# Kernel tuning notes

Measured on AMD Instinct MI355X. Metric: run time of the kernel, lower is better.

Reference implementation:

```python
import jax, jax.numpy as jnp
import numpy as np

B = 4
C = 128           # input channels
H = W = 512       # image size
P = 16            # patch size
GH = GW = 32      # token grid (H//P, W//P)
N = GH * GW       # num patches = 1024
PATCH_DIM = C * P * P  # 32768
DIM = 512         # embed dim
MLP = 256         # ffn hidden
DH = 64           # dim per head
HEADS = (2, 4, 8) # per-layer head counts
NUM_REL = (2 * GH - 1) * (2 * GW - 1)  # 3969


def _rel_index():
    # faithful to the torch buffer construction (meshgrid default 'ij')
    coords = np.stack(np.meshgrid(np.arange(GH), np.arange(GW), indexing='ij')).reshape(2, -1)
    rc = (coords[:, :, None] - coords[:, None, :]).transpose(1, 2, 0)  # [N,N,2]
    rc[..., 0] += GH - 1
    rc[..., 1] += GW - 1
    rc[..., 0] *= 2 * GH - 1
    return jnp.asarray(rc.sum(-1))  # [N,N] int

REL_IDX = _rel_index()


def _ln(x, s, b):
    m = x.mean(-1, keepdims=True)
    v = x.var(-1, keepdims=True)
    return (x - m) / jnp.sqrt(v + 1e-5) * s + b


def setup_inputs() -> dict:
    key = jax.random.key(0)
    ks = iter(jax.random.split(key, 40))
    def rn(shape, scale=0.02):
        return jax.random.normal(next(ks), shape, jnp.float32) * scale
    inp = {"img": jax.random.normal(next(ks), (B, C, H, W), jnp.float32)}
    inp["patch_w"] = rn((PATCH_DIM, DIM))
    inp["patch_b"] = jnp.zeros((DIM,), jnp.float32)
    inp["pos_emb"] = rn((1, N, DIM), 1.0)
    inp["ln1_s"] = jnp.ones((3, DIM), jnp.float32)
    inp["ln1_b"] = jnp.zeros((3, DIM), jnp.float32)
    inp["ln2_s"] = jnp.ones((3, DIM), jnp.float32)
    inp["ln2_b"] = jnp.zeros((3, DIM), jnp.float32)
    for l, h in enumerate(HEADS):
        inner = DH * h
        inp[f"qkv_w{l}"] = rn((DIM, 3 * inner))
        inp[f"out_w{l}"] = rn((inner, DIM))
        inp[f"out_b{l}"] = jnp.zeros((DIM,), jnp.float32)
        inp[f"bias{l}"] = rn((NUM_REL, h))
    inp["ff_w1"] = rn((3, DIM, MLP))
    inp["ff_b1"] = jnp.zeros((3, MLP), jnp.float32)
    inp["ff_w2"] = rn((3, MLP, DIM))
    inp["ff_b2"] = jnp.zeros((3, DIM), jnp.float32)
    return inp


def reference(img, patch_w, patch_b, pos_emb, ln1_s, ln1_b, ln2_s, ln2_b,
              qkv_w0, qkv_w1, qkv_w2, out_w0, out_w1, out_w2,
              out_b0, out_b1, out_b2, bias0, bias1, bias2,
              ff_w1, ff_b1, ff_w2, ff_b2):
    b = img.shape[0]
    # Rearrange 'b c (h p1) (w p2) -> b (h w) (p1 p2 c)'
    x = img.reshape(b, C, GH, P, GW, P).transpose(0, 2, 4, 3, 5, 1).reshape(b, N, PATCH_DIM)
    x = x @ patch_w + patch_b + pos_emb

    qkv_ws = (qkv_w0, qkv_w1, qkv_w2)
    out_ws = (out_w0, out_w1, out_w2)
    out_bs = (out_b0, out_b1, out_b2)
    tables = (bias0, bias1, bias2)

    for l, h in enumerate(HEADS):
        # attention with relative position bias
        xn = _ln(x, ln1_s[l], ln1_b[l])
        qkv = xn @ qkv_ws[l]                                  # [b, N, 3*h*DH]
        q, k, v = jnp.split(qkv, 3, axis=-1)
        q = q.reshape(b, N, h, DH).transpose(0, 2, 1, 3)      # bhnd
        k = k.reshape(b, N, h, DH).transpose(0, 2, 1, 3)
        v = v.reshape(b, N, h, DH).transpose(0, 2, 1, 3)
        dots = jnp.einsum('bhnd,bhmd->bhnm', q, k) * (DH ** -0.5)
        rel = tables[l][REL_IDX].transpose(2, 0, 1)           # [h, N, N]
        attn = jax.nn.softmax(dots + rel[None], axis=-1)
        o = jnp.einsum('bhnm,bhmd->bhnd', attn, v)
        o = o.transpose(0, 2, 1, 3).reshape(b, N, h * DH)
        x = o @ out_ws[l] + out_bs[l] + x
        # feed-forward
        xn = _ln(x, ln2_s[l], ln2_b[l])
        hmid = jax.nn.gelu(xn @ ff_w1[l] + ff_b1[l], approximate=False)
        x = hmid @ ff_w2[l] + ff_b2[l] + x

    return x.transpose(0, 2, 1).reshape(b, DIM, GH, GW)
```

## Files before the change

kernel.cpp:

```cpp
#include <hip/hip_runtime.h>

typedef unsigned short u16;
typedef __bf16 bf16x8 __attribute__((ext_vector_type(8)));
typedef float f32x4 __attribute__((ext_vector_type(4)));

#define AS1 __attribute__((address_space(1)))
#define AS3 __attribute__((address_space(3)))
#define MFMA(a,b,c) __builtin_amdgcn_mfma_f32_16x16x32_bf16(a,b,c,0,0,0)

__device__ __forceinline__ u16 f2bf(float f) {
    union { float f; unsigned u; } x; x.f = f;
    unsigned r = x.u + 0x7fffu + ((x.u >> 16) & 1u);
    return (u16)(r >> 16);
}

__global__ void k_patch_wT(const float* __restrict__ w, u16* __restrict__ o)
{
    __shared__ u16 T[256*33];
    int c = blockIdx.x, n0 = blockIdx.y*32;
    int t = threadIdx.x;
    int rr = t >> 5, cc = t & 31;
    #pragma unroll
    for (int i = 0; i < 32; ++i) {
        int r = i*8 + rr;
        int k = (r >> 4)*2048 + (r & 15)*128 + c;
        T[r*33 + cc] = f2bf(w[(size_t)k*512 + n0 + cc]);
    }
    __syncthreads();
    #pragma unroll
    for (int i = 0; i < 4; ++i) {
        int j  = i*8 + (t >> 5);
        int ch = t & 31;
        union { u16 u[8]; uint4 v; } pk;
        #pragma unroll
        for (int q = 0; q < 8; ++q) pk.u[q] = T[(ch*8+q)*33 + j];
        *(uint4*)(o + (size_t)(n0 + j)*32768 + c*256 + ch*8) = pk.v;
    }
}

__global__ void k_init_x(float* __restrict__ x, const float* __restrict__ pb, const float* __restrict__ pe)
{
    int i4 = blockIdx.x*256 + threadIdx.x;
    size_t base = (size_t)i4*4;
    float4 a = *(const float4*)(pb + (base & 511));
    float4 b = *(const float4*)(pe + (base & 524287));
    float4 r = make_float4(a.x+b.x, a.y+b.y, a.z+b.z, a.w+b.w);
    *(float4*)(x + base) = r;
}

struct TXJob { const float* in; u16* out; int K, N, tiles; };
struct TXArgs { TXJob j[12]; };

__global__ void k_wT_all(TXArgs a)
{
    __shared__ float T[32*33];
    int bid = blockIdx.x;
    int ji = 0;
    while (bid >= a.j[ji].tiles) { bid -= a.j[ji].tiles; ++ji; }
    const float* __restrict__ in = a.j[ji].in;
    u16* __restrict__ o = a.j[ji].out;
    const int K = a.j[ji].K, N = a.j[ji].N;
    const int tn = N >> 5;
    const int kt = (bid / tn) * 32, nt = (bid % tn) * 32;
    int t = threadIdx.x, r = t >> 5, c = t & 31;
    #pragma unroll
    for (int i = 0; i < 4; ++i)
        T[(r + i*8)*33 + c] = in[(size_t)(kt + r + i*8)*N + nt + c];
    __syncthreads();
    #pragma unroll
    for (int i = 0; i < 4; ++i)
        o[(size_t)(nt + r + i*8)*K + kt + c] = f2bf(T[c*33 + r + i*8]);
}

__global__ __launch_bounds__(1024) void k_patch_gemm(
    const float* __restrict__ img, const u16* __restrict__ Bt, float* __restrict__ Cf)
{
    __shared__ alignas(16) u16 As[2*128*64];
    __shared__ alignas(16) u16 Bs[2*512*64];
    const int t = threadIdx.x;
    const int bid = blockIdx.x;
    const int z = bid & 7;
    const int tile = bid >> 3;
    const int b = tile >> 3, gh0 = (tile & 7)*4;
    const int m0 = tile*128;
    const int wave = t >> 6, lane = t & 63;
    const int r16 = lane & 15, g = lane >> 4;
    const int wm = (wave >> 3)*64, wn = (wave & 7)*64;

    const int arow = t >> 6;
    const int ghl = arow >> 2, p1l = arow & 3;
    const int aw = (t & 63)*8;
    const int tok = ghl*32 + (aw >> 4);
    unsigned abyte = (unsigned)(tok*128 + p1l*32 + (aw & 15)*2);
    abyte ^= (unsigned)((tok & 7) << 4);
    const float* imgb = img + (size_t)b*128*262144
                      + (size_t)((gh0 + ghl)*16 + p1l)*512 + aw;
    const int brow = t >> 3;
    const int bchunk = (t & 7) ^ (brow & 7);
    const u16* Bb = Bt + (size_t)brow*32768 + (size_t)z*4096 + bchunk*8;
    u16* Bsd = Bs + t*8;

    f32x4 acc[4][4];
    const f32x4 zz = {0.f,0.f,0.f,0.f};
    #pragma unroll
    for (int im = 0; im < 4; ++im)
        #pragma unroll
        for (int in_ = 0; in_ < 4; ++in_) acc[im][in_] = zz;

#define ALOAD(R0, R1, KC) do {                                                       \
    const int c_ = z*16 + ((KC) >> 2);                                               \
    const float* s_ = imgb + (size_t)c_*262144 + ((KC) & 3)*2048;                    \
    R0 = *(const float4*)s_;  R1 = *(const float4*)(s_ + 4); } while(0)
#define AWRITE(R0, R1, BUF) do {                                                     \
    union { u16 u[8]; uint4 v; } pk_;                                                \
    pk_.u[0]=f2bf(R0.x); pk_.u[1]=f2bf(R0.y); pk_.u[2]=f2bf(R0.z); pk_.u[3]=f2bf(R0.w); \
    pk_.u[4]=f2bf(R1.x); pk_.u[5]=f2bf(R1.y); pk_.u[6]=f2bf(R1.z); pk_.u[7]=f2bf(R1.w); \
    *(uint4*)((char*)As + (BUF)*16384 + abyte) = pk_.v; } while(0)
#define BSTAGE(KC, BUF) do { _Pragma("unroll")                                       \
    for (int i_ = 0; i_ < 4; ++i_)                                                   \
        __builtin_amdgcn_global_load_lds((AS1 void*)(Bb + (size_t)i_*128*32768 + (KC)*64), \
                                         (AS3 void*)(Bsd + (BUF)*32768 + i_*8192), 16, 0, 0); } while(0)

    float4 e0, e1;
    ALOAD(e0, e1, 0);
    BSTAGE(0, 0);
    AWRITE(e0, e1, 0);
    __syncthreads();
    int cur = 0;
    for (int kc = 0; kc < 64; ++kc) {
        if (kc < 63) {
            ALOAD(e0, e1, kc + 1);
            BSTAGE(kc + 1, cur ^ 1);
        }
        const char* Asb = (const char*)As + cur*16384;
        const char* Bsb = (const char*)Bs + cur*65536;
        #pragma unroll
        for (int kk = 0; kk < 64; kk += 32) {
            bf16x8 af[4], bfr[4];
            #pragma unroll
            for (int im = 0; im < 4; ++im) {
                unsigned off = ((unsigned)((wm + im*16 + r16)*128 + kk*2 + g*16))
                             ^ (unsigned)((r16 & 7) << 4);
                af[im] = *(const bf16x8*)(Asb + off);
            }
            #pragma unroll
            for (int in_ = 0; in_ < 4; ++in_) {
                unsigned off = ((unsigned)((wn + in_*16 + r16)*128 + kk*2 + g*16))
                             ^ (unsigned)((r16 & 7) << 4);
                bfr[in_] = *(const bf16x8*)(Bsb + off);
            }
            #pragma unroll
            for (int im = 0; im < 4; ++im)
                #pragma unroll
                for (int in_ = 0; in_ < 4; ++in_)
                    acc[im][in_] = MFMA(af[im], bfr[in_], acc[im][in_]);
        }
        if (kc < 63) AWRITE(e0, e1, cur ^ 1);
        __syncthreads();
        cur ^= 1;
    }
#undef ALOAD
#undef AWRITE
#undef BSTAGE
    #pragma unroll
    for (int im = 0; im < 4; ++im) {
        int row = m0 + wm + im*16 + g*4;
        #pragma unroll
        for (int in_ = 0; in_ < 4; ++in_) {
            int col = wn + in_*16 + r16;
            #pragma unroll
            for (int r = 0; r < 4; ++r)
                __hip_atomic_fetch_add(&Cf[(size_t)(row + r)*512 + col], acc[im][in_][r],
                                       __ATOMIC_RELAXED, __HIP_MEMORY_SCOPE_AGENT);
        }
    }
}

__global__ void k_ln(const float* __restrict__ x, const float* __restrict__ sc,
                     const float* __restrict__ bi, u16* __restrict__ o)
{
    int row = blockIdx.x, lane = threadIdx.x;
    const float* xr = x + (size_t)row*512 + lane*8;
    float4 v0 = *(const float4*)xr;
    float4 v1 = *(const float4*)(xr + 4);
    float vv[8] = {v0.x,v0.y,v0.z,v0.w,v1.x,v1.y,v1.z,v1.w};
    float sum = 0.f, sq = 0.f;
    #pragma unroll
    for (int i = 0; i < 8; ++i) { sum += vv[i]; sq += vv[i]*vv[i]; }
    #pragma unroll
    for (int m = 1; m < 64; m <<= 1) { sum += __shfl_xor(sum, m, 64); sq += __shfl_xor(sq, m, 64); }
    float mean = sum * (1.f/512.f);
    float var  = sq  * (1.f/512.f) - mean*mean;
    float rstd = rsqrtf(var + 1e-5f);
    int d = lane*8;
    union { u16 u[8]; uint4 v; } pk;
    #pragma unroll
    for (int i = 0; i < 8; ++i) pk.u[i] = f2bf((vv[i]-mean)*rstd*sc[d+i] + bi[d+i]);
    *(uint4*)(o + (size_t)row*512 + d) = pk.v;
}

template<int EPI, int KB>
__global__ __launch_bounds__(256) void k_gemm(
    const u16* __restrict__ A, int lda,
    const u16* __restrict__ Bt, int ldb,
    float* __restrict__ Cf, u16* __restrict__ Cb, int ldc,
    const float* __restrict__ bias)
{
    __shared__ alignas(16) u16 As[128*64];
    __shared__ alignas(16) u16 Bs[128*64];
    const int t = threadIdx.x;
    const int m0 = blockIdx.x*128, n0 = blockIdx.y*128;
    const int wave = t >> 6, lane = t & 63;
    const int wm = (wave >> 1)*64, wn = (wave & 1)*64;
    const int r16 = lane & 15, g = lane >> 4;
    const u16* Ab = A + (size_t)(m0 + (t>>3))*lda + (t&7)*8;
    const u16* Bb = Bt + (size_t)(n0 + (t>>3))*ldb + (t&7)*8;
    u16* Asd = As + t*8;
    u16* Bsd = Bs + t*8;
    f32x4 acc[4][4];
    const f32x4 z4 = {0.f,0.f,0.f,0.f};
    #pragma unroll
    for (int im = 0; im < 4; ++im)
        #pragma unroll
        for (int in_ = 0; in_ < 4; ++in_) acc[im][in_] = z4;

    #pragma unroll
    for (int k = 0; k < KB; k += 64) {
        #pragma unroll
        for (int i = 0; i < 4; ++i) {
            __builtin_amdgcn_global_load_lds((AS1 void*)(Ab + (size_t)i*32*lda + k), (AS3 void*)(Asd + i*2048), 16, 0, 0);
            __builtin_amdgcn_global_load_lds((AS1 void*)(Bb + (size_t)i*32*ldb + k), (AS3 void*)(Bsd + i*2048), 16, 0, 0);
        }
        __syncthreads();
        #pragma unroll
        for (int kk = 0; kk < 64; kk += 32) {
            bf16x8 af[4], bfr[4];
            #pragma unroll
            for (int im = 0; im < 4; ++im)
                af[im] = *(const bf16x8*)(As + (wm + im*16 + r16)*64 + kk + g*8);
            #pragma unroll
            for (int in_ = 0; in_ < 4; ++in_)
                bfr[in_] = *(const bf16x8*)(Bs + (wn + in_*16 + r16)*64 + kk + g*8);
            #pragma unroll
            for (int im = 0; im < 4; ++im)
                #pragma unroll
                for (int in_ = 0; in_ < 4; ++in_)
                    acc[im][in_] = MFMA(af[im], bfr[in_], acc[im][in_]);
        }
        __syncthreads();
    }
    #pragma unroll
    for (int im = 0; im < 4; ++im) {
        int row = m0 + wm + im*16 + g*4;
        #pragma unroll
        for (int in_ = 0; in_ < 4; ++in_) {
            int col = n0 + wn + in_*16 + r16;
            #pragma unroll
            for (int r = 0; r < 4; ++r) {
                float v = acc[im][in_][r];
                size_t idx = (size_t)(row + r)*ldc + col;
                if constexpr (EPI == 1) {
                    Cb[idx] = f2bf(v);
                } else if constexpr (EPI == 2) {
                    float xv = v + bias[col];
                    Cb[idx] = f2bf(0.5f*xv*(1.f + erff(xv*0.70710678118654752f)));
                } else {
                    Cf[idx] += v + bias[col];
                }
            }
        }
    }
}

__global__ __launch_bounds__(256) void k_attn(
    const u16* __restrict__ qkv, const float* __restrict__ bt,
    u16* __restrict__ o, int H)
{
    const int LD = 80;
    __shared__ alignas(16) u16 Qs[64*80], Ks[64*80], Vs[64*80];
    __shared__ alignas(16) u16 Ps[4][16*80];
    const int inner = H*64, s3 = 3*inner;
    const int qt = blockIdx.x, head = blockIdx.y, b = blockIdx.z;
    const int t = threadIdx.x, wave = t >> 6, lane = t & 63;
    const int r16 = lane & 15, g = lane >> 4;
    const int q0 = qt*64;
    const size_t tokbase = (size_t)b*1024;
    const int hoff = head*64;

    #pragma unroll
    for (int it = 0; it < 2; ++it) {
        int flat = it*256 + t, r = flat >> 3, d0 = (flat & 7)*8;
        uint4 v = *(const uint4*)(qkv + (tokbase + q0 + r)*s3 + hoff + d0);
        *(uint4*)(Qs + r*LD + d0) = v;
    }
    __syncthreads();
    bf16x8 aQ0 = *(const bf16x8*)(Qs + (wave*16 + r16)*LD + g*8);
    bf16x8 aQ1 = *(const bf16x8*)(Qs + (wave*16 + r16)*LD + 32 + g*8);

    float m_[4], l_[4];
    f32x4 O[4];
    const f32x4 z4 = {0.f,0.f,0.f,0.f};
    #pragma unroll
    for (int r = 0; r < 4; ++r) { m_[r] = -1e30f; l_[r] = 0.f; O[r] = z4; }
    const int qg_base = q0 + wave*16 + g*4;

    for (int kt = 0; kt < 16; ++kt) {
        const int key0 = kt*64;
        #pragma unroll
        for (int it = 0; it < 2; ++it) {
            int flat = it*256 + t, r = flat >> 3, d0 = (flat & 7)*8;
            uint4 v = *(const uint4*)(qkv + (tokbase + key0 + r)*s3 + inner + hoff + d0);
            *(uint4*)(Ks + r*LD + d0) = v;
        }
        #pragma unroll
        for (int it = 0; it < 2; ++it) {
            int flat = it*256 + t, key = flat & 63, d0 = (flat >> 6)*8;
            uint4 v = *(const uint4*)(qkv + (tokbase + key0 + key)*s3 + 2*inner + hoff + d0);
            const u16* pv = (const u16*)&v;
            #pragma unroll
            for (int i = 0; i < 8; ++i) Vs[(d0+i)*LD + key] = pv[i];
        }
        __syncthreads();

        float Sv[4][4];
        #pragma unroll
        for (int kb = 0; kb < 4; ++kb) {
            bf16x8 k0f = *(const bf16x8*)(Ks + (kb*16 + r16)*LD + g*8);
            bf16x8 k1f = *(const bf16x8*)(Ks + (kb*16 + r16)*LD + 32 + g*8);
            f32x4 S = z4;
            S = MFMA(aQ0, k0f, S);
            S = MFMA(aQ1, k1f, S);
            int keyg = key0 + kb*16 + r16;
            int kgh = keyg >> 5, kgw = keyg & 31;
            #pragma unroll
            for (int r = 0; r < 4; ++r) {
                int qg = qg_base + r;
                int rel = ((qg >> 5) - kgh + 31)*63 + ((qg & 31) - kgw + 31);
                Sv[kb][r] = S[r]*0.125f + bt[rel*H + head];
            }
        }
        float mx[4], al[4], ps[4];
        #pragma unroll
        for (int r = 0; r < 4; ++r)
            mx[r] = fmaxf(fmaxf(Sv[0][r], Sv[1][r]), fmaxf(Sv[2][r], Sv[3][r]));
        #pragma unroll
        for (int msk = 1; msk < 16; msk <<= 1)
            #pragma unroll
            for (int r = 0; r < 4; ++r) mx[r] = fmaxf(mx[r], __shfl_xor(mx[r], msk, 64));
        #pragma unroll
        for (int r = 0; r < 4; ++r) {
            float nm = fmaxf(m_[r], mx[r]);
            al[r] = __expf(m_[r] - nm);
            m_[r] = nm;
            ps[r] = 0.f;
        }
        #pragma unroll
        for (int kb = 0; kb < 4; ++kb)
            #pragma unroll
            for (int r = 0; r < 4; ++r) {
                float p = __expf(Sv[kb][r] - m_[r]);
                Sv[kb][r] = p;
                ps[r] += p;
            }
        #pragma unroll
        for (int msk = 1; msk < 16; msk <<= 1)
            #pragma unroll
            for (int r = 0; r < 4; ++r) ps[r] += __shfl_xor(ps[r], msk, 64);
        #pragma unroll
        for (int r = 0; r < 4; ++r) l_[r] = l_[r]*al[r] + ps[r];
        #pragma unroll
        for (int kb = 0; kb < 4; ++kb)
            #pragma unroll
            for (int r = 0; r < 4; ++r)
                Ps[wave][(g*4 + r)*LD + kb*16 + r16] = f2bf(Sv[kb][r]);
        #pragma unroll
        for (int dt = 0; dt < 4; ++dt)
            #pragma unroll
            for (int r = 0; r < 4; ++r) O[dt][r] = O[dt][r]*al[r];
        __syncthreads();
        bf16x8 aP0 = *(const bf16x8*)(Ps[wave] + r16*LD + g*8);
        bf16x8 aP1 = *(const bf16x8*)(Ps[wave] + r16*LD + 32 + g*8);
        #pragma unroll
        for (int dt = 0; dt < 4; ++dt) {
            bf16x8 v0 = *(const bf16x8*)(Vs + (dt*16 + r16)*LD + g*8);
            bf16x8 v1 = *(const bf16x8*)(Vs + (dt*16 + r16)*LD + 32 + g*8);
            O[dt] = MFMA(aP0, v0, O[dt]);
            O[dt] = MFMA(aP1, v1, O[dt]);
        }
        __syncthreads();
    }
    #pragma unroll
    for (int dt = 0; dt < 4; ++dt)
        #pragma unroll
        for (int r = 0; r < 4; ++r) {
            int token = q0 + wave*16 + g*4 + r;
            o[(tokbase + token)*inner + hoff + dt*16 + r16] = f2bf(O[dt][r] / l_[r]);
        }
}

__global__ void k_out_transpose(const float* __restrict__ x, float* __restrict__ o)
{
    __shared__ float T[32*33];
    int d0 = blockIdx.x*32, n0 = blockIdx.y*32, b = blockIdx.z;
    int t = threadIdx.x, r = t >> 5, c = t & 31;
    #pragma unroll
    for (int i = 0; i < 4; ++i)
        T[(r+i*8)*33 + c] = x[((size_t)b*1024 + n0 + r + i*8)*512 + d0 + c];
    __syncthreads();
    #pragma unroll
    for (int i = 0; i < 4; ++i)
        o[((size_t)b*512 + d0 + r + i*8)*1024 + n0 + c] = T[c*33 + (r+i*8)];
}

extern "C" void kernel_launch(void* const* d_in, const int* in_sizes, int n_in,
                              void* d_out, int out_size, void* d_ws, size_t ws_size,
                              hipStream_t stream)
{
    (void)in_sizes; (void)n_in; (void)out_size; (void)ws_size;
    const float* img     = (const float*)d_in[0];
    const float* patch_w = (const float*)d_in[1];
    const float* patch_b = (const float*)d_in[2];
    const float* pos_emb = (const float*)d_in[3];
    const float* ln1_s   = (const float*)d_in[4];
    const float* ln1_b   = (const float*)d_in[5];
    const float* ln2_s   = (const float*)d_in[6];
    const float* ln2_b   = (const float*)d_in[7];
    const float* qkv_w[3] = {(const float*)d_in[8],  (const float*)d_in[12], (const float*)d_in[16]};
    const float* out_w[3] = {(const float*)d_in[9],  (const float*)d_in[13], (const float*)d_in[17]};
    const float* out_b[3] = {(const float*)d_in[10], (const float*)d_in[14], (const float*)d_in[18]};
    const float* biasT[3] = {(const float*)d_in[11], (const float*)d_in[15], (const float*)d_in[19]};
    const float* ff_w1 = (const float*)d_in[20];
    const float* ff_b1 = (const float*)d_in[21];
    const float* ff_w2 = (const float*)d_in[22];
    const float* ff_b2 = (const float*)d_in[23];
    float* out = (float*)d_out;

    const int HS[3] = {2, 4, 8};

    char* ws = (char*)d_ws;
    size_t off = 0;
    auto alloc = [&](size_t bytes) -> void* {
        void* p = ws + off; off += (bytes + 255) & ~(size_t)255; return p;
    };
    u16*   pwT  = (u16*)  alloc(512ull*32768*2);
    float* x    = (float*)alloc(4096ull*512*4);
    u16*   xn   = (u16*)  alloc(4096ull*512*2);
    u16*   qkv  = (u16*)  alloc(4096ull*1536*2);
    u16*   ob   = (u16*)  alloc(4096ull*512*2);
    u16*   mid  = (u16*)  alloc(4096ull*256*2);
    u16*   qkvT = (u16*)  alloc(2688ull*512*2);
    u16*   outT = (u16*)  alloc(512ull*896*2);
    u16*   f1T  = (u16*)  alloc(3ull*256*512*2);
    u16*   f2T  = (u16*)  alloc(3ull*512*256*2);

    u16* qkvT_l[3] = { qkvT, qkvT + 384ull*512, qkvT + (384ull+768)*512 };
    u16* outT_l[3] = { outT, outT + 512ull*128, outT + 512ull*(128+256) };
    u16* f1T_l[3]  = { f1T,  f1T  + 256ull*512, f1T  + 2ull*256*512 };
    u16* f2T_l[3]  = { f2T,  f2T  + 512ull*256, f2T  + 2ull*512*256 };

    k_patch_wT<<<dim3(128,16), 256, 0, stream>>>(patch_w, pwT);
    k_init_x<<<2048, 256, 0, stream>>>(x, patch_b, pos_emb);

    TXArgs tx;
    int tj = 0, total_tiles = 0;
    auto add_job = [&](const float* in, u16* o, int K, int N) {
        tx.j[tj] = TXJob{in, o, K, N, (K/32)*(N/32)};
        total_tiles += tx.j[tj].tiles; ++tj;
    };
    for (int l = 0; l < 3; ++l) add_job(qkv_w[l], qkvT_l[l], 512, 3*64*HS[l]);
    for (int l = 0; l < 3; ++l) add_job(out_w[l], outT_l[l], 64*HS[l], 512);
    for (int l = 0; l < 3; ++l) add_job(ff_w1 + (size_t)l*512*256, f1T_l[l], 512, 256);
    for (int l = 0; l < 3; ++l) add_job(ff_w2 + (size_t)l*256*512, f2T_l[l], 256, 512);
    k_wT_all<<<total_tiles, 256, 0, stream>>>(tx);

    k_patch_gemm<<<256, 1024, 0, stream>>>(img, pwT, x);

    for (int l = 0; l < 3; ++l) {
        int h = HS[l], inner = 64*h, n3 = 3*inner;

        k_ln<<<4096, 64, 0, stream>>>(x, ln1_s + l*512, ln1_b + l*512, xn);
        k_gemm<1,512><<<dim3(32, n3/128), 256, 0, stream>>>(xn, 512, qkvT_l[l], 512,
                                                            nullptr, qkv, n3, nullptr);
        k_attn<<<dim3(16, h, 4), 256, 0, stream>>>(qkv, biasT[l], ob, h);
        if (l == 0)
            k_gemm<3,128><<<dim3(32, 4), 256, 0, stream>>>(ob, inner, outT_l[l], inner,
                                                           x, nullptr, 512, out_b[l]);
        else if (l == 1)
            k_gemm<3,256><<<dim3(32, 4), 256, 0, stream>>>(ob, inner, outT_l[l], inner,
                                                           x, nullptr, 512, out_b[l]);
        else
            k_gemm<3,512><<<dim3(32, 4), 256, 0, stream>>>(ob, inner, outT_l[l], inner,
                                                           x, nullptr, 512, out_b[l]);
        k_ln<<<4096, 64, 0, stream>>>(x, ln2_s + l*512, ln2_b + l*512, xn);
        k_gemm<2,512><<<dim3(32, 2), 256, 0, stream>>>(xn, 512, f1T_l[l], 512,
                                                       nullptr, mid, 256, ff_b1 + l*256);
        k_gemm<3,256><<<dim3(32, 4), 256, 0, stream>>>(mid, 256, f2T_l[l], 256,
                                                       x, nullptr, 512, ff_b2 + l*512);
    }
    k_out_transpose<<<dim3(16, 32, 4), 256, 0, stream>>>(x, out);
}
```

Baseline: 742.2 us.

## Prefetch patch-embed GEMM tiles two stages ahead with explicit vmcnt waits

Restructures the patch-embedding GEMM main loop so global loads for stage kc+2 are issued right after the barrier, with manual s_waitcnt vmcnt/lgkmcnt and s_barrier in place of __syncthreads. B tiles stream into LDS while older loads are still outstanding. This aims to hide global memory latency behind the MFMA work. The hand-counted vmcnt values are easy to get wrong, and the B async LDS loads and A register loads share the same counter.

```diff
diff --git a/kernel.cpp b/kernel.cpp
--- a/kernel.cpp
+++ b/kernel.cpp
@@ -107,31 +107,36 @@
         #pragma unroll
         for (int in_ = 0; in_ < 4; ++in_) acc[im][in_] = zz;
 
-#define ALOAD(R0, R1, KC) do {                                                       \
+#define ALOAD(KC) do {                                                               \
     const int c_ = z*16 + ((KC) >> 2);                                               \
     const float* s_ = imgb + (size_t)c_*262144 + ((KC) & 3)*2048;                    \
-    R0 = *(const float4*)s_;  R1 = *(const float4*)(s_ + 4); } while(0)
-#define AWRITE(R0, R1, BUF) do {                                                     \
+    e0 = *(const float4*)s_;  e1 = *(const float4*)(s_ + 4); } while(0)
+#define AWRITE(BUF) do {                                                             \
     union { u16 u[8]; uint4 v; } pk_;                                                \
-    pk_.u[0]=f2bf(R0.x); pk_.u[1]=f2bf(R0.y); pk_.u[2]=f2bf(R0.z); pk_.u[3]=f2bf(R0.w); \
-    pk_.u[4]=f2bf(R1.x); pk_.u[5]=f2bf(R1.y); pk_.u[6]=f2bf(R1.z); pk_.u[7]=f2bf(R1.w); \
+    pk_.u[0]=f2bf(e0.x); pk_.u[1]=f2bf(e0.y); pk_.u[2]=f2bf(e0.z); pk_.u[3]=f2bf(e0.w); \
+    pk_.u[4]=f2bf(e1.x); pk_.u[5]=f2bf(e1.y); pk_.u[6]=f2bf(e1.z); pk_.u[7]=f2bf(e1.w); \
     *(uint4*)((char*)As + (BUF)*16384 + abyte) = pk_.v; } while(0)
 #define BSTAGE(KC, BUF) do { _Pragma("unroll")                                       \
     for (int i_ = 0; i_ < 4; ++i_)                                                   \
         __builtin_amdgcn_global_load_lds((AS1 void*)(Bb + (size_t)i_*128*32768 + (KC)*64), \
                                          (AS3 void*)(Bsd + (BUF)*32768 + i_*8192), 16, 0, 0); } while(0)
+#define WAITVM(N) asm volatile("s_waitcnt vmcnt(" #N ")" ::: "memory")
+#define WAITLG   asm volatile("s_waitcnt lgkmcnt(0)" ::: "memory")
 
     float4 e0, e1;
-    ALOAD(e0, e1, 0);
+    ALOAD(0);
     BSTAGE(0, 0);
-    AWRITE(e0, e1, 0);
-    __syncthreads();
+    WAITVM(4);
+    AWRITE(0);
+    ALOAD(1);
+    BSTAGE(1, 1);
+    WAITLG;
+    WAITVM(6);
+    __builtin_amdgcn_s_barrier();
+    __builtin_amdgcn_sched_barrier(0);
+
     int cur = 0;
     for (int kc = 0; kc < 64; ++kc) {
-        if (kc < 63) {
-            ALOAD(e0, e1, kc + 1);
-            BSTAGE(kc + 1, cur ^ 1);
-        }
         const char* Asb = (const char*)As + cur*16384;
         const char* Bsb = (const char*)Bs + cur*65536;
         #pragma unroll
@@ -155,13 +160,27 @@
                 for (int in_ = 0; in_ < 4; ++in_)
                     acc[im][in_] = MFMA(af[im], bfr[in_], acc[im][in_]);
         }
-        if (kc < 63) AWRITE(e0, e1, cur ^ 1);
-        __syncthreads();
+        if (kc < 63) {
+            WAITVM(4);
+            AWRITE(cur ^ 1);
+        }
+        WAITLG;
+        __builtin_amdgcn_s_barrier();
+        if (kc < 62) {
+            ALOAD(kc + 2);
+            BSTAGE(kc + 2, cur);
+            WAITVM(6);
+        } else {
+            WAITVM(0);
+        }
+        __builtin_amdgcn_sched_barrier(0);
         cur ^= 1;
     }
 #undef ALOAD
 #undef AWRITE
 #undef BSTAGE
+#undef WAITVM
+#undef WAITLG
     #pragma unroll
     for (int im = 0; im < 4; ++im) {
         int row = m0 + wm + im*16 + g*4;
```

Result: no change. 735.2 us (-1.0%).
